# Kernel optimization log

Measured on AMD Instinct MI355X. Metric: run time of the kernel, lower is better.

The kernel has to match this reference:

```python
import jax, jax.numpy as jnp
import numpy as np

EMBED_DIM = 768
NUM_HEADS = 12
HEAD_DIM = EMBED_DIM // NUM_HEADS
IMG_LEN = 196
TXT_LEN = 1852
SEQ_LEN = IMG_LEN + TXT_LEN
BATCH = 4
NEG = -1e9


def setup_inputs() -> dict:
    key = jax.random.key(0)
    ks = jax.random.split(key, 10)
    s = 1.0 / np.sqrt(EMBED_DIM)
    return {
        "x": jax.random.normal(ks[0], (BATCH, SEQ_LEN, EMBED_DIM), jnp.float32),
        "input_padding_mask": jax.random.randint(ks[1], (BATCH, TXT_LEN), 0, 2, jnp.int32),
        "Wq": jax.random.normal(ks[2], (EMBED_DIM, EMBED_DIM), jnp.float32) * s,
        "bq": jax.random.normal(ks[3], (EMBED_DIM,), jnp.float32) * 0.01,
        "Wk": jax.random.normal(ks[4], (EMBED_DIM, EMBED_DIM), jnp.float32) * s,
        "bk": jax.random.normal(ks[5], (EMBED_DIM,), jnp.float32) * 0.01,
        "Wv": jax.random.normal(ks[6], (EMBED_DIM, EMBED_DIM), jnp.float32) * s,
        "bv": jax.random.normal(ks[7], (EMBED_DIM,), jnp.float32) * 0.01,
        "Wo": jax.random.normal(ks[8], (EMBED_DIM, EMBED_DIM), jnp.float32) * s,
        "bo": jax.random.normal(ks[9], (EMBED_DIM,), jnp.float32) * 0.01,
    }


def _prefix_causal_mask():
    # tril ones, but all rows fully attend to the image prefix columns
    m = jnp.tril(jnp.ones((SEQ_LEN, SEQ_LEN), jnp.float32))
    m = m.at[:, :IMG_LEN].set(1.0)
    return m


def reference(x, input_padding_mask, Wq, bq, Wk, bk, Wv, bv, Wo, bo):
    B, S, E = x.shape
    H, D = NUM_HEADS, HEAD_DIM
    # torch nn.Linear: y = x @ W.T + b, weight shape [out, in]
    q = (x @ Wq.T + bq).reshape(B, S, H, D).transpose(0, 2, 1, 3)  # [B,H,S,D]
    k = (x @ Wk.T + bk).reshape(B, S, H, D).transpose(0, 2, 1, 3)
    v = (x @ Wv.T + bv).reshape(B, S, H, D).transpose(0, 2, 1, 3)

    sims = jnp.einsum("bhqd,bhkd->bhqk", q, k) / jnp.sqrt(jnp.float32(D))
    mask = _prefix_causal_mask()[None, None]  # [1,1,S,S]
    sims = jnp.where(mask == 0, NEG, sims)

    # padding mask over key positions (image prefix always valid)
    full_pad = jnp.concatenate(
        [jnp.ones((B, IMG_LEN), input_padding_mask.dtype), input_padding_mask], axis=1
    )  # [B,S]
    sims = jnp.where(full_pad[:, None, None, :] == 0, NEG, sims)

    attn = jax.nn.softmax(sims, axis=-1)
    out = jnp.einsum("bhqk,bhkd->bhqd", attn, v)
    out = out.transpose(0, 2, 1, 3).reshape(B, S, E)
    return out @ Wo.T + bo
```

## Files before the change

### kernel.cpp

```cpp
#include <hip/hip_runtime.h>

#define B_ 4
#define S_ 2048
#define E_ 768
#define H_ 12
#define D_ 64
#define IMG_ 196
#define TXT_ 1852
#define NEG_ (-1e9f)
#define QSCALE_ 0.18033688f
#define SMAX_ 8.0f
#define EXP2_(x) __builtin_amdgcn_exp2f(x)

typedef __bf16 bf16x8 __attribute__((ext_vector_type(8)));
typedef float f32x4 __attribute__((ext_vector_type(4)));
typedef float f32x16 __attribute__((ext_vector_type(16)));

__device__ __forceinline__ unsigned short f2b(float f) {
    __bf16 h = (__bf16)f;
    return __builtin_bit_cast(unsigned short, h);
}
__device__ __forceinline__ unsigned int pack2(float lo, float hi) {
    return (unsigned int)f2b(lo) | ((unsigned int)f2b(hi) << 16);
}
__device__ __forceinline__ void gload16(const unsigned short* g, unsigned short* l) {
    __builtin_amdgcn_global_load_lds(
        (const __attribute__((address_space(1))) unsigned int*)g,
        (__attribute__((address_space(3))) unsigned int*)l, 16, 0, 0);
}


__global__ __launch_bounds__(256) void cvt_kernel(const float* __restrict__ src,
                                                  unsigned short* __restrict__ dst,
                                                  int n4) {
    int i = blockIdx.x * 256 + threadIdx.x;
    if (i < n4) {
        float4 f = reinterpret_cast<const float4*>(src)[i];
        ushort4 u;
        u.x = f2b(f.x); u.y = f2b(f.y); u.z = f2b(f.z); u.w = f2b(f.w);
        reinterpret_cast<ushort4*>(dst)[i] = u;
    }
}

__global__ __launch_bounds__(256) void cvtw_kernel(
    const float* __restrict__ w0, const float* __restrict__ w1,
    const float* __restrict__ w2, const float* __restrict__ w3,
    unsigned short* __restrict__ d0, unsigned short* __restrict__ d1,
    unsigned short* __restrict__ d2, unsigned short* __restrict__ d3,
    int n4) {
    int i = blockIdx.x * 256 + threadIdx.x;
    if (i >= n4) return;
    int which = blockIdx.y;
    const float* src = (which == 0) ? w0 : (which == 1) ? w1 : (which == 2) ? w2 : w3;
    unsigned short* dst = (which == 0) ? d0 : (which == 1) ? d1 : (which == 2) ? d2 : d3;
    float4 f = reinterpret_cast<const float4*>(src)[i];
    ushort4 u;
    u.x = f2b(f.x); u.y = f2b(f.y); u.z = f2b(f.z); u.w = f2b(f.w);
    reinterpret_cast<ushort4*>(dst)[i] = u;
}

__global__ __launch_bounds__(256) void padneg_kernel(const int* __restrict__ pad,
                                                     float* __restrict__ padneg) {
    int i = blockIdx.x * 256 + threadIdx.x;
    if (i < B_ * S_) {
        int b = i >> 11, s = i & 2047;
        float v = -SMAX_;
        if (s >= IMG_ && pad[b * TXT_ + (s - IMG_)] == 0) v = NEG_;
        padneg[i] = v;
    }
}

__global__ __launch_bounds__(256) void qkv_gemm(
    const unsigned short* __restrict__ xb,
    const unsigned short* __restrict__ wqb,
    const unsigned short* __restrict__ wkb,
    const unsigned short* __restrict__ wvb,
    const float* __restrict__ bq, const float* __restrict__ bk,
    const float* __restrict__ bv,
    unsigned short* __restrict__ qfb, unsigned short* __restrict__ kfb,
    unsigned short* __restrict__ vfb)
{
    __shared__ __align__(16) unsigned short As[128 * 64];
    __shared__ __align__(16) unsigned short Bs[128 * 64];
    const int m0 = blockIdx.x * 128;
    const int n0 = blockIdx.y * 128;
    const int which = n0 / E_;
    const int ncol0 = n0 % E_;
    const unsigned short* W = (which == 0) ? wqb : ((which == 1) ? wkb : wvb);
    const int t = threadIdx.x;
    const int lane = t & 63, wid = t >> 6;
    const int wr = wid >> 1, wc = wid & 1;
    const int c = lane & 15, g = lane >> 4;
    const int srow = lane >> 3;
    const int sslot = (lane & 7) ^ srow;

    f32x4 acc[4][4];
#pragma unroll
    for (int i = 0; i < 4; ++i)
#pragma unroll
        for (int j = 0; j < 4; ++j) acc[i][j] = (f32x4){0.f, 0.f, 0.f, 0.f};

    for (int k0 = 0; k0 < E_; k0 += 64) {
        __syncthreads();
#pragma unroll
        for (int j = 0; j < 8; ++j) {
            int chunk = wid * 8 + j;
            int isB = chunk >> 4;
            int ch = chunk & 15;
            int row = ch * 8 + srow;
            const unsigned short* src =
                (isB ? W + (size_t)(ncol0 + row) * E_
                     : xb + (size_t)(m0 + row) * E_) + k0 + sslot * 8;
            unsigned short* dst = (isB ? Bs : As) + ch * 512;
            gload16(src, dst);
        }
        __syncthreads();

        bf16x8 af[2][4], bfv[2][4];
#pragma unroll
        for (int kk = 0; kk < 2; ++kk) {
#pragma unroll
            for (int fr = 0; fr < 4; ++fr) {
                int row = wr * 64 + fr * 16 + c;
                af[kk][fr] = *reinterpret_cast<const bf16x8*>(
                    &As[row * 64 + (((kk * 4 + g) ^ (row & 7)) * 8)]);
            }
#pragma unroll
            for (int fc = 0; fc < 4; ++fc) {
                int row = wc * 64 + fc * 16 + c;
                bfv[kk][fc] = *reinterpret_cast<const bf16x8*>(
                    &Bs[row * 64 + (((kk * 4 + g) ^ (row & 7)) * 8)]);
            }
        }
#pragma unroll
        for (int kk = 0; kk < 2; ++kk)
#pragma unroll
            for (int fr = 0; fr < 4; ++fr)
#pragma unroll
                for (int fc = 0; fc < 4; ++fc)
                    acc[fr][fc] = __builtin_amdgcn_mfma_f32_16x16x32_bf16(
                        af[kk][fr], bfv[kk][fc], acc[fr][fc], 0, 0, 0);
    }

    const float* bias_ptr = (which == 0) ? bq : ((which == 1) ? bk : bv);
    if (which != 2) {
        unsigned short* dstbuf = (which == 0) ? qfb : kfb;
        const float oscale = (which == 0) ? QSCALE_ : 1.0f;
#pragma unroll
        for (int fc = 0; fc < 4; ++fc) {
            int e = ncol0 + wc * 64 + fc * 16 + c;
            float bias = bias_ptr[e];
            int hd = e >> 6, d = e & 63;
            int dc = d >> 4, hf = (d >> 3) & 1, e8 = d & 7;
#pragma unroll
            for (int fr = 0; fr < 4; ++fr) {
#pragma unroll
                for (int r = 0; r < 4; ++r) {
                    int m = m0 + wr * 64 + fr * 16 + g * 4 + r;
                    int b = m >> 11, s = m & 2047;
                    int bh = b * H_ + hd, t32 = s >> 5, sl = s & 31;
                    size_t off = ((((size_t)bh * 64 + t32) * 4 + dc) * 64
                                  + hf * 32 + sl) * 8 + e8;
                    dstbuf[off] = f2b((acc[fr][fc][r] + bias) * oscale);
                }
            }
        }
    } else {
#pragma unroll
        for (int fc = 0; fc < 4; ++fc) {
            int e = ncol0 + wc * 64 + fc * 16 + c;
            float bias = bias_ptr[e];
            int hd = e >> 6, d = e & 63;
            int vh = d >> 5, dl = d & 31;
#pragma unroll
            for (int fr = 0; fr < 4; ++fr) {
                int m = m0 + wr * 64 + fr * 16 + g * 4;
                int b = m >> 11, s = m & 2047;
                int bh = b * H_ + hd, t32 = s >> 5, ks = s & 31;
                int mm = ks >> 4, hb = (ks >> 3) & 1;
                int e8 = (ks & 7) ^ ((ks & 8) >> 1);
                size_t off = (((((size_t)bh * 64 + t32) * 2 + mm) * 2 + vh) * 64
                              + hb * 32 + dl) * 8 + e8;
                uint2 pk;
                pk.x = pack2(acc[fr][fc][0] + bias, acc[fr][fc][1] + bias);
                pk.y = pack2(acc[fr][fc][2] + bias, acc[fr][fc][3] + bias);
                *reinterpret_cast<uint2*>(&vfb[off]) = pk;
            }
        }
    }
}

__global__ __launch_bounds__(256) void attn_kernel(
    const unsigned short* __restrict__ qF,
    const unsigned short* __restrict__ kF,
    const unsigned short* __restrict__ vF,
    const float* __restrict__ padneg,
    unsigned short* __restrict__ ob)
{
    __shared__ float exch[3][33 * 64];
    const int flat = blockIdx.x;
    const int xcd = flat & 7, idx = flat >> 3;
    const int bh = xcd * 6 + (idx >> 6);
    const int qt = 63 - (idx & 63);
    const int b = bh / H_, hh = bh % H_;
    const int t = threadIdx.x;
    const int lane = t & 63, w = t >> 6;
    const int h = lane >> 5, ql = lane & 31;
    const int qbase = qt * 32;
    const int q = qbase + ql;
    const float* pn2 = padneg + b * S_ + 4 * h;

    bf16x8 qf[4];
    {
        const unsigned short* qp = qF + ((size_t)(bh * 64 + qt) * 4) * 512 + lane * 8;
#pragma unroll
        for (int dc = 0; dc < 4; ++dc)
            qf[dc] = *reinterpret_cast<const bf16x8*>(qp + dc * 512);
    }

    f32x16 oa0, oa1;
#pragma unroll
    for (int r = 0; r < 16; ++r) { oa0[r] = 0.f; oa1[r] = 0.f; }
    float lr = 0.f;

    int kmax = qbase + 32; if (kmax < IMG_) kmax = IMG_;
    const int nt = (kmax + 31) >> 5;
    const int cchunk = (nt + 3) >> 2;
    const int t0w = w * cchunk;
    const int t1w = min(nt, t0w + cchunk);
    const bool hasC = (t1w == nt) && (t0w < t1w);
    const int preEnd = hasC ? (t1w - 1) : t1w;

    const unsigned short* kbase = kF + ((size_t)bh * 64 * 4) * 512 + lane * 8;
    const unsigned short* vbase = vF + ((size_t)bh * 64 * 4) * 512 + lane * 8;

    auto pvstep = [&](const f32x16& p, const bf16x8 (&vf)[4]) {
        unsigned int pka0 = pack2(p[0], p[1]),   pkb0 = pack2(p[2], p[3]);
        unsigned int pka1 = pack2(p[4], p[5]),   pkb1 = pack2(p[6], p[7]);
        unsigned int pka2 = pack2(p[8], p[9]),   pkb2 = pack2(p[10], p[11]);
        unsigned int pka3 = pack2(p[12], p[13]), pkb3 = pack2(p[14], p[15]);
#pragma unroll
        for (int m = 0; m < 2; ++m) {
            unsigned int keep0 = h ? (m ? pka3 : pka1) : (m ? pka2 : pka0);
            unsigned int keep1 = h ? (m ? pkb3 : pkb1) : (m ? pkb2 : pkb0);
            unsigned int send0 = h ? (m ? pka2 : pka0) : (m ? pka3 : pka1);
            unsigned int send1 = h ? (m ? pkb2 : pkb0) : (m ? pkb3 : pkb1);
            unsigned int x0 = (unsigned int)__shfl_xor((int)send0, 32, 64);
            unsigned int x1 = (unsigned int)__shfl_xor((int)send1, 32, 64);
            uint4 fr;
            fr.x = keep0;
            fr.y = keep1;
            fr.z = x0;
            fr.w = x1;
            bf16x8 pb = __builtin_bit_cast(bf16x8, fr);
            oa0 = __builtin_amdgcn_mfma_f32_32x32x16_bf16(vf[2 * m + 0], pb, oa0, 0, 0, 0);
            oa1 = __builtin_amdgcn_mfma_f32_32x32x16_bf16(vf[2 * m + 1], pb, oa1, 0, 0, 0);
        }
    };

    int kt = t0w;
    for (; kt + 2 <= preEnd; kt += 2) {
        const unsigned short* kpa = kbase + (size_t)kt * 2048;
        bf16x8 ka[4], kb4[4];
#pragma unroll
        for (int dc = 0; dc < 4; ++dc) {
            ka[dc]  = *reinterpret_cast<const bf16x8*>(kpa + dc * 512);
            kb4[dc] = *reinterpret_cast<const bf16x8*>(kpa + 2048 + dc * 512);
        }
        f32x16 sa, sb;
#pragma unroll
        for (int r = 0; r < 16; ++r) { sa[r] = 0.f; sb[r] = 0.f; }
#pragma unroll
        for (int dc = 0; dc < 4; ++dc) {
            sa = __builtin_amdgcn_mfma_f32_32x32x16_bf16(ka[dc],  qf[dc], sa, 0, 0, 0);
            sb = __builtin_amdgcn_mfma_f32_32x32x16_bf16(kb4[dc], qf[dc], sb, 0, 0, 0);
        }
        bf16x8 va[4], vb[4];
        {
            const unsigned short* vpa = vbase + (size_t)kt * 2048;
#pragma unroll
            for (int j = 0; j < 4; ++j) {
                va[j] = *reinterpret_cast<const bf16x8*>(vpa + j * 512);
                vb[j] = *reinterpret_cast<const bf16x8*>(vpa + 2048 + j * 512);
            }
        }
        const float* pp = pn2 + kt * 32;
        float pna[16], pnb[16];
#pragma unroll
        for (int gg = 0; gg < 4; ++gg) {
            *reinterpret_cast<float4*>(&pna[4 * gg]) =
                *reinterpret_cast<const float4*>(pp + gg * 8);
            *reinterpret_cast<float4*>(&pnb[4 * gg]) =
                *reinterpret_cast<const float4*>(pp + 32 + gg * 8);
        }
#pragma unroll
        for (int r = 0; r < 16; ++r) {
            sa[r] = EXP2_(sa[r] + pna[r]);
            sb[r] = EXP2_(sb[r] + pnb[r]);
        }
        float u0 = (sa[0] + sa[1]) + (sa[2] + sa[3]);
        float u1 = (sa[4] + sa[5]) + (sa[6] + sa[7]);
        float u2 = (sa[8] + sa[9]) + (sa[10] + sa[11]);
        float u3 = (sa[12] + sa[13]) + (sa[14] + sa[15]);
        float v0 = (sb[0] + sb[1]) + (sb[2] + sb[3]);
        float v1 = (sb[4] + sb[5]) + (sb[6] + sb[7]);
        float v2 = (sb[8] + sb[9]) + (sb[10] + sb[11]);
        float v3 = (sb[12] + sb[13]) + (sb[14] + sb[15]);
        lr += ((u0 + u1) + (u2 + u3)) + ((v0 + v1) + (v2 + v3));
        pvstep(sa, va);
        pvstep(sb, vb);
    }

#pragma unroll 1
    for (int pass = (kt < preEnd) ? 0 : 1; pass < (hasC ? 2 : 1); ++pass) {
        const int tile = pass ? (nt - 1) : kt;
        const bool causal = (pass == 1);
        const unsigned short* kp = kbase + (size_t)tile * 2048;
        bf16x8 kf4[4];
#pragma unroll
        for (int dc = 0; dc < 4; ++dc)
            kf4[dc] = *reinterpret_cast<const bf16x8*>(kp + dc * 512);
        f32x16 s;
#pragma unroll
        for (int r = 0; r < 16; ++r) s[r] = 0.f;
#pragma unroll
        for (int dc = 0; dc < 4; ++dc)
            s = __builtin_amdgcn_mfma_f32_32x32x16_bf16(kf4[dc], qf[dc], s, 0, 0, 0);
        bf16x8 vt[4];
        {
            const unsigned short* vp = vbase + (size_t)tile * 2048;
#pragma unroll
            for (int j = 0; j < 4; ++j)
                vt[j] = *reinterpret_cast<const bf16x8*>(vp + j * 512);
        }
        const int k0 = tile * 32;
        float pna[16];
#pragma unroll
        for (int gg = 0; gg < 4; ++gg)
            *reinterpret_cast<float4*>(&pna[4 * gg]) =
                *reinterpret_cast<const float4*>(pn2 + k0 + gg * 8);
#pragma unroll
        for (int r = 0; r < 16; ++r) s[r] += pna[r];
        if (causal) {
#pragma unroll
            for (int r = 0; r < 16; ++r) {
                int key = k0 + (r & 3) + 8 * (r >> 2) + 4 * h;
                if (!((key <= q) || (key < IMG_))) s[r] = NEG_;
            }
        }
#pragma unroll
        for (int r = 0; r < 16; ++r) s[r] = EXP2_(s[r]);
        float u0 = (s[0] + s[1]) + (s[2] + s[3]);
        float u1 = (s[4] + s[5]) + (s[6] + s[7]);
        float u2 = (s[8] + s[9]) + (s[10] + s[11]);
        float u3 = (s[12] + s[13]) + (s[14] + s[15]);
        lr += (u0 + u1) + (u2 + u3);
        pvstep(s, vt);
    }

    if (w > 0) {
        float* X = exch[w - 1];
#pragma unroll
        for (int r = 0; r < 16; ++r) {
            X[r * 64 + lane] = oa0[r];
            X[(16 + r) * 64 + lane] = oa1[r];
        }
        X[32 * 64 + lane] = lr;
    }
    __syncthreads();
    if (w > 0) return;

    float L = lr;
#pragma unroll
    for (int i = 0; i < 3; ++i) {
        L += exch[i][32 * 64 + lane];
#pragma unroll
        for (int r = 0; r < 16; ++r) {
            oa0[r] += exch[i][r * 64 + lane];
            oa1[r] += exch[i][(16 + r) * 64 + lane];
        }
    }
    L += __shfl_xor(L, 32, 64);

    float inv = 1.f / L;
    unsigned short* orow = ob + ((size_t)(b * S_ + q)) * E_ + hh * D_;
#pragma unroll
    for (int gg = 0; gg < 4; ++gg) {
        int d0 = gg * 8 + 4 * h;
        uint2 s0, s1;
        s0.x = pack2(oa0[4 * gg] * inv, oa0[4 * gg + 1] * inv);
        s0.y = pack2(oa0[4 * gg + 2] * inv, oa0[4 * gg + 3] * inv);
        s1.x = pack2(oa1[4 * gg] * inv, oa1[4 * gg + 1] * inv);
        s1.y = pack2(oa1[4 * gg + 2] * inv, oa1[4 * gg + 3] * inv);
        *reinterpret_cast<uint2*>(orow + d0) = s0;
        *reinterpret_cast<uint2*>(orow + 32 + d0) = s1;
    }
}

__global__ __launch_bounds__(256) void oproj_gemm(
    const unsigned short* __restrict__ ab,
    const unsigned short* __restrict__ wob,
    const float* __restrict__ bo,
    float* __restrict__ out)
{
    __shared__ __align__(16) unsigned short As[128 * 64];
    __shared__ __align__(16) unsigned short Bs[128 * 64];
    const int m0 = blockIdx.x * 128;
    const int n0 = blockIdx.y * 128;
    const int t = threadIdx.x;
    const int lane = t & 63, wid = t >> 6;
    const int wr = wid >> 1, wc = wid & 1;
    const int c = lane & 15, g = lane >> 4;
    const int srow = lane >> 3;
    const int sslot = (lane & 7) ^ srow;

    f32x4 acc[4][4];
#pragma unroll
    for (int i = 0; i < 4; ++i)
#pragma unroll
        for (int j = 0; j < 4; ++j) acc[i][j] = (f32x4){0.f, 0.f, 0.f, 0.f};

    for (int k0 = 0; k0 < E_; k0 += 64) {
        __syncthreads();
#pragma unroll
        for (int j = 0; j < 8; ++j) {
            int chunk = wid * 8 + j;
            int isB = chunk >> 4;
            int ch = chunk & 15;
            int row = ch * 8 + srow;
            const unsigned short* src =
                (isB ? wob + (size_t)(n0 + row) * E_
                     : ab + (size_t)(m0 + row) * E_) + k0 + sslot * 8;
            unsigned short* dst = (isB ? Bs : As) + ch * 512;
            gload16(src, dst);
        }
        __syncthreads();

        bf16x8 af[2][4], bfv[2][4];
#pragma unroll
        for (int kk = 0; kk < 2; ++kk) {
#pragma unroll
            for (int fr = 0; fr < 4; ++fr) {
                int row = wr * 64 + fr * 16 + c;
                af[kk][fr] = *reinterpret_cast<const bf16x8*>(
                    &As[row * 64 + (((kk * 4 + g) ^ (row & 7)) * 8)]);
            }
#pragma unroll
            for (int fc = 0; fc < 4; ++fc) {
                int row = wc * 64 + fc * 16 + c;
                bfv[kk][fc] = *reinterpret_cast<const bf16x8*>(
                    &Bs[row * 64 + (((kk * 4 + g) ^ (row & 7)) * 8)]);
            }
        }
#pragma unroll
        for (int kk = 0; kk < 2; ++kk)
#pragma unroll
            for (int fr = 0; fr < 4; ++fr)
#pragma unroll
                for (int fc = 0; fc < 4; ++fc)
                    acc[fr][fc] = __builtin_amdgcn_mfma_f32_16x16x32_bf16(
                        af[kk][fr], bfv[kk][fc], acc[fr][fc], 0, 0, 0);
    }

#pragma unroll
    for (int fc = 0; fc < 4; ++fc) {
        int n = n0 + wc * 64 + fc * 16 + c;
        float bias = bo[n];
#pragma unroll
        for (int fr = 0; fr < 4; ++fr)
#pragma unroll
            for (int r = 0; r < 4; ++r) {
                int m = m0 + wr * 64 + fr * 16 + g * 4 + r;
                out[(size_t)m * E_ + n] = acc[fr][fc][r] + bias;
            }
    }
}

extern "C" void kernel_launch(void* const* d_in, const int* in_sizes, int n_in,
                              void* d_out, int out_size, void* d_ws, size_t ws_size,
                              hipStream_t stream) {
    const float* x  = (const float*)d_in[0];
    const int* pad  = (const int*)d_in[1];
    const float* Wq = (const float*)d_in[2];
    const float* bq = (const float*)d_in[3];
    const float* Wk = (const float*)d_in[4];
    const float* bk = (const float*)d_in[5];
    const float* Wv = (const float*)d_in[6];
    const float* bv = (const float*)d_in[7];
    const float* Wo = (const float*)d_in[8];
    const float* bo = (const float*)d_in[9];
    float* out = (float*)d_out;

    const size_t NX = (size_t)B_ * S_ * E_;
    const size_t NW = (size_t)E_ * E_;
    unsigned short* ws = (unsigned short*)d_ws;
    unsigned short* xb  = ws;
    unsigned short* wqb = xb + NX;
    unsigned short* wkb = wqb + NW;
    unsigned short* wvb = wkb + NW;
    unsigned short* wob = wvb + NW;
    unsigned short* qfb = wob + NW;
    unsigned short* kfb = qfb + NX;
    unsigned short* vfb = kfb + NX;
    unsigned short* obuf = vfb + NX;
    float* padneg = (float*)(obuf + NX);

    cvt_kernel<<<(int)(NX / 4 / 256), 256, 0, stream>>>(x, xb, (int)(NX / 4));
    cvtw_kernel<<<dim3((int)(NW / 4 / 256), 4), 256, 0, stream>>>(
        Wq, Wk, Wv, Wo, wqb, wkb, wvb, wob, (int)(NW / 4));
    padneg_kernel<<<(B_ * S_) / 256, 256, 0, stream>>>(pad, padneg);

    qkv_gemm<<<dim3(64, 18), 256, 0, stream>>>(xb, wqb, wkb, wvb, bq, bk, bv,
                                               qfb, kfb, vfb);
    attn_kernel<<<dim3(3072), 256, 0, stream>>>(qfb, kfb, vfb, padneg, obuf);
    oproj_gemm<<<dim3(64, 6), 256, 0, stream>>>(obuf, wob, bo, out);
}
```

Baseline: 149.9 us.

## Double-buffer LDS tiles with BK=32 in QKV and output projection GEMMs

Both projection GEMMs now stage K-slices of 32 into two LDS buffers, issuing the next slice's global-to-LDS loads before computing on the current one, so there is one barrier per step instead of two. The LDS layout and swizzle are reorganized for 16-row chunks of 32 columns. This is meant to hide global load latency behind MFMA work. It doubles the number of loop iterations and relies on the direct-to-LDS loads having completed at the barrier without an explicit vmcnt wait, which could be a correctness risk.

```diff
diff --git a/kernel.cpp b/kernel.cpp
--- a/kernel.cpp
+++ b/kernel.cpp
@@ -28,6 +28,7 @@
         (const __attribute__((address_space(1))) unsigned int*)g,
         (__attribute__((address_space(3))) unsigned int*)l, 16, 0, 0);
 }
+
 
 
 __global__ __launch_bounds__(256) void cvt_kernel(const float* __restrict__ src,
@@ -80,8 +81,7 @@
     unsigned short* __restrict__ qfb, unsigned short* __restrict__ kfb,
     unsigned short* __restrict__ vfb)
 {
-    __shared__ __align__(16) unsigned short As[128 * 64];
-    __shared__ __align__(16) unsigned short Bs[128 * 64];
+    __shared__ __align__(16) unsigned short SB[16384];
     const int m0 = blockIdx.x * 128;
     const int n0 = blockIdx.y * 128;
     const int which = n0 / E_;
@@ -91,8 +91,20 @@
     const int lane = t & 63, wid = t >> 6;
     const int wr = wid >> 1, wc = wid & 1;
     const int c = lane & 15, g = lane >> 4;
-    const int srow = lane >> 3;
-    const int sslot = (lane & 7) ^ srow;
+    const int sr = lane >> 3, s8 = lane & 7;
+    const int u = s8 ^ sr, hi = u >> 2, c8 = u & 3;
+    const unsigned short* gsrc[4];
+    int ldoff[4];
+#pragma unroll
+    for (int j = 0; j < 4; ++j) {
+        int ch = wid * 4 + j;
+        int isB = ch >> 3, chm = ch & 7;
+        int row = chm * 16 + sr * 2 + hi;
+        gsrc[j] = (isB ? W + (size_t)(ncol0 + row) * E_
+                       : xb + (size_t)(m0 + row) * E_) + c8 * 8;
+        ldoff[j] = isB * 4096 + chm * 512;
+    }
+    const int rdoff = (c >> 1) * 64 + (((((c & 1) << 2) | g)) ^ (c >> 1)) * 8;
 
     f32x4 acc[4][4];
 #pragma unroll
@@ -100,47 +112,36 @@
 #pragma unroll
         for (int j = 0; j < 4; ++j) acc[i][j] = (f32x4){0.f, 0.f, 0.f, 0.f};
 
-    for (int k0 = 0; k0 < E_; k0 += 64) {
+    auto COMPUTE = [&](int curv) {
+        const unsigned short* Ab = SB + curv * 8192;
+        bf16x8 af[4], bfv[4];
+#pragma unroll
+        for (int fr = 0; fr < 4; ++fr)
+            af[fr] = *reinterpret_cast<const bf16x8*>(Ab + (wr * 4 + fr) * 512 + rdoff);
+#pragma unroll
+        for (int fc = 0; fc < 4; ++fc)
+            bfv[fc] = *reinterpret_cast<const bf16x8*>(Ab + 4096 + (wc * 4 + fc) * 512 + rdoff);
+#pragma unroll
+        for (int fr = 0; fr < 4; ++fr)
+#pragma unroll
+            for (int fc = 0; fc < 4; ++fc)
+                acc[fr][fc] = __builtin_amdgcn_mfma_f32_16x16x32_bf16(
+                    af[fr], bfv[fc], acc[fr][fc], 0, 0, 0);
+    };
+
+#pragma unroll
+    for (int j = 0; j < 4; ++j) gload16(gsrc[j], SB + ldoff[j]);
+    __syncthreads();
+    int cur = 0;
+    for (int tt = 0; tt < 23; ++tt) {
+        const int nb = (cur ^ 1) * 8192, nco = (tt + 1) * 32;
+#pragma unroll
+        for (int j = 0; j < 4; ++j) gload16(gsrc[j] + nco, SB + nb + ldoff[j]);
+        COMPUTE(cur);
         __syncthreads();
-#pragma unroll
-        for (int j = 0; j < 8; ++j) {
-            int chunk = wid * 8 + j;
-            int isB = chunk >> 4;
-            int ch = chunk & 15;
-            int row = ch * 8 + srow;
-            const unsigned short* src =
-                (isB ? W + (size_t)(ncol0 + row) * E_
-                     : xb + (size_t)(m0 + row) * E_) + k0 + sslot * 8;
-            unsigned short* dst = (isB ? Bs : As) + ch * 512;
-            gload16(src, dst);
-        }
-        __syncthreads();
-
-        bf16x8 af[2][4], bfv[2][4];
-#pragma unroll
-        for (int kk = 0; kk < 2; ++kk) {
-#pragma unroll
-            for (int fr = 0; fr < 4; ++fr) {
-                int row = wr * 64 + fr * 16 + c;
-                af[kk][fr] = *reinterpret_cast<const bf16x8*>(
-                    &As[row * 64 + (((kk * 4 + g) ^ (row & 7)) * 8)]);
-            }
-#pragma unroll
-            for (int fc = 0; fc < 4; ++fc) {
-                int row = wc * 64 + fc * 16 + c;
-                bfv[kk][fc] = *reinterpret_cast<const bf16x8*>(
-                    &Bs[row * 64 + (((kk * 4 + g) ^ (row & 7)) * 8)]);
-            }
-        }
-#pragma unroll
-        for (int kk = 0; kk < 2; ++kk)
-#pragma unroll
-            for (int fr = 0; fr < 4; ++fr)
-#pragma unroll
-                for (int fc = 0; fc < 4; ++fc)
-                    acc[fr][fc] = __builtin_amdgcn_mfma_f32_16x16x32_bf16(
-                        af[kk][fr], bfv[kk][fc], acc[fr][fc], 0, 0, 0);
-    }
+        cur ^= 1;
+    }
+    COMPUTE(cur);
 
     const float* bias_ptr = (which == 0) ? bq : ((which == 1) ? bk : bv);
     if (which != 2) {
@@ -403,16 +404,27 @@
     const float* __restrict__ bo,
     float* __restrict__ out)
 {
-    __shared__ __align__(16) unsigned short As[128 * 64];
-    __shared__ __align__(16) unsigned short Bs[128 * 64];
+    __shared__ __align__(16) unsigned short SB[16384];
     const int m0 = blockIdx.x * 128;
     const int n0 = blockIdx.y * 128;
     const int t = threadIdx.x;
     const int lane = t & 63, wid = t >> 6;
     const int wr = wid >> 1, wc = wid & 1;
     const int c = lane & 15, g = lane >> 4;
-    const int srow = lane >> 3;
-    const int sslot = (lane & 7) ^ srow;
+    const int sr = lane >> 3, s8 = lane & 7;
+    const int u = s8 ^ sr, hi = u >> 2, c8 = u & 3;
+    const unsigned short* gsrc[4];
+    int ldoff[4];
+#pragma unroll
+    for (int j = 0; j < 4; ++j) {
+        int ch = wid * 4 + j;
+        int isB = ch >> 3, chm = ch & 7;
+        int row = chm * 16 + sr * 2 + hi;
+        gsrc[j] = (isB ? wob + (size_t)(n0 + row) * E_
+                       : ab + (size_t)(m0 + row) * E_) + c8 * 8;
+        ldoff[j] = isB * 4096 + chm * 512;
+    }
+    const int rdoff = (c >> 1) * 64 + (((((c & 1) << 2) | g)) ^ (c >> 1)) * 8;
 
     f32x4 acc[4][4];
 #pragma unroll
@@ -420,47 +432,36 @@
 #pragma unroll
         for (int j = 0; j < 4; ++j) acc[i][j] = (f32x4){0.f, 0.f, 0.f, 0.f};
 
-    for (int k0 = 0; k0 < E_; k0 += 64) {
+    auto COMPUTE = [&](int curv) {
+        const unsigned short* Ab = SB + curv * 8192;
+        bf16x8 af[4], bfv[4];
+#pragma unroll
+        for (int fr = 0; fr < 4; ++fr)
+            af[fr] = *reinterpret_cast<const bf16x8*>(Ab + (wr * 4 + fr) * 512 + rdoff);
+#pragma unroll
+        for (int fc = 0; fc < 4; ++fc)
+            bfv[fc] = *reinterpret_cast<const bf16x8*>(Ab + 4096 + (wc * 4 + fc) * 512 + rdoff);
+#pragma unroll
+        for (int fr = 0; fr < 4; ++fr)
+#pragma unroll
+            for (int fc = 0; fc < 4; ++fc)
+                acc[fr][fc] = __builtin_amdgcn_mfma_f32_16x16x32_bf16(
+                    af[fr], bfv[fc], acc[fr][fc], 0, 0, 0);
+    };
+
+#pragma unroll
+    for (int j = 0; j < 4; ++j) gload16(gsrc[j], SB + ldoff[j]);
+    __syncthreads();
+    int cur = 0;
+    for (int tt = 0; tt < 23; ++tt) {
+        const int nb = (cur ^ 1) * 8192, nco = (tt + 1) * 32;
+#pragma unroll
+        for (int j = 0; j < 4; ++j) gload16(gsrc[j] + nco, SB + nb + ldoff[j]);
+        COMPUTE(cur);
         __syncthreads();
-#pragma unroll
-        for (int j = 0; j < 8; ++j) {
-            int chunk = wid * 8 + j;
-            int isB = chunk >> 4;
-            int ch = chunk & 15;
-            int row = ch * 8 + srow;
-            const unsigned short* src =
-                (isB ? wob + (size_t)(n0 + row) * E_
-                     : ab + (size_t)(m0 + row) * E_) + k0 + sslot * 8;
-            unsigned short* dst = (isB ? Bs : As) + ch * 512;
-            gload16(src, dst);
-        }
-        __syncthreads();
-
-        bf16x8 af[2][4], bfv[2][4];
-#pragma unroll
-        for (int kk = 0; kk < 2; ++kk) {
-#pragma unroll
-            for (int fr = 0; fr < 4; ++fr) {
-                int row = wr * 64 + fr * 16 + c;
-                af[kk][fr] = *reinterpret_cast<const bf16x8*>(
-                    &As[row * 64 + (((kk * 4 + g) ^ (row & 7)) * 8)]);
-            }
-#pragma unroll
-            for (int fc = 0; fc < 4; ++fc) {
-                int row = wc * 64 + fc * 16 + c;
-                bfv[kk][fc] = *reinterpret_cast<const bf16x8*>(
-                    &Bs[row * 64 + (((kk * 4 + g) ^ (row & 7)) * 8)]);
-            }
-        }
-#pragma unroll
-        for (int kk = 0; kk < 2; ++kk)
-#pragma unroll
-            for (int fr = 0; fr < 4; ++fr)
-#pragma unroll
-                for (int fc = 0; fc < 4; ++fc)
-                    acc[fr][fc] = __builtin_amdgcn_mfma_f32_16x16x32_bf16(
-                        af[kk][fr], bfv[kk][fc], acc[fr][fc], 0, 0, 0);
-    }
+        cur ^= 1;
+    }
+    COMPUTE(cur);
 
 #pragma unroll
     for (int fc = 0; fc < 4; ++fc) {
```

Result: no change. 152.6 us (+1.8%).
